# Kernel optimization log

Measured on AMD Instinct MI355X. Metric: run time of the kernel, lower is better.

The kernel has to match this reference:

```python
import jax, jax.numpy as jnp
import numpy as np

N = 100000   # nodes
E = 1000000  # edges
D = 64       # in_features
D_OUT = 64   # out_features


def setup_inputs() -> dict:
    key = jax.random.key(0)
    k1, k2, k3, k4, k5, k6 = jax.random.split(key, 6)
    h = jax.random.normal(k1, (N, D), dtype=jnp.float32)          # current node features ndata['h']
    i = jax.random.normal(k2, (N, D), dtype=jnp.float32)          # initial features ndata['i']
    edge_src = jax.random.randint(k3, (E,), 0, N, dtype=jnp.int32)
    edge_dst = jax.random.randint(k4, (E,), 0, N, dtype=jnp.int32)
    edge_w = jax.random.uniform(k5, (E,), dtype=jnp.float32)      # scalar edge weight edata['x']
    stdv = 1.0 / np.sqrt(D_OUT)
    weight = jax.random.uniform(k6, (2 * D, D_OUT), dtype=jnp.float32,
                                minval=-stdv, maxval=stdv)        # variant=True -> in = 2*D
    return {
        "h": h, "i": i, "weight": weight, "edge_w": edge_w,
        "lamda": jnp.float32(0.5), "alpha": jnp.float32(0.1),
        "edge_src": edge_src, "edge_dst": edge_dst, "layer_idx": 4,
    }


def reference(h, i, weight, edge_w, lamda, alpha, edge_src, edge_dst, layer_idx):
    # theta = min(1, log(lamda/layer_idx + 1))
    theta = jnp.minimum(jnp.float32(1.0), jnp.log(lamda / layer_idx + 1.0))
    # update_all(u_mul_e('h','x','m'), sum('m','h')): edge-weighted gather-scatter SpMM
    m = h[edge_src] * edge_w[:, None]                 # [E, D]
    h_agg = jax.ops.segment_sum(m, edge_dst, num_segments=h.shape[0])  # [N, D]
    # variant=True branch
    support = jnp.concatenate([h_agg, i], axis=1)     # [N, 2D]
    r = (1.0 - alpha) * h_agg + alpha * i             # [N, D]
    out = theta * (support @ weight) + (1.0 - theta) * r
    # residual=True
    out = out + i
    return out
```

## Files before the change

### kernel.cpp

```cpp
#include <hip/hip_runtime.h>
#include <hip/hip_fp16.h>
#include <math.h>


#define DFEAT 64
#define BINSZ 64
#define NBINS 2048
#define CAP   1024
#define CHUNK 2048
#define EPT   4
#define TPB   512

#define ASTR  72

typedef unsigned long long u64;
typedef __attribute__((ext_vector_type(8))) _Float16 f16x8;
typedef __attribute__((ext_vector_type(4))) float f32x4;

__device__ inline unsigned h2u(__half2 h) {
    union { __half2 h; unsigned u; } c; c.h = h; return c.u;
}
__device__ inline __half2 u2h(unsigned u) {
    union { unsigned u; __half2 h; } c; c.u = u; return c.h;
}

__global__ __launch_bounds__(256) void convert_kernel(
    const float* __restrict__ h, const float* __restrict__ weight,
    ushort* __restrict__ h16, ushort* __restrict__ w16,
    int* __restrict__ gcur, int total4) {
    int gid = blockIdx.x * 256 + threadIdx.x;
    int nth = gridDim.x * 256;
    if (gid < NBINS) gcur[gid] = 0;
    for (int i = gid; i < total4; i += nth) {
        float4 v = ((const float4*)h)[i];
        uint2 o;
        o.x = h2u(__floats2half2_rn(v.x, v.y));
        o.y = h2u(__floats2half2_rn(v.z, v.w));
        ((uint2*)h16)[i] = o;
    }
    if (gid < 8192) {
        int j = gid & 7, l = (gid >> 3) & 63, cs = gid >> 9;
        int c = cs >> 2, s = cs & 3, q = l >> 4, m = l & 15;
        w16[gid] = __half_as_ushort(
            __float2half_rn(weight[(s * 32 + q * 8 + j) * DFEAT + c * 16 + m]));
    }
}

__global__ __launch_bounds__(512) void bin_fill_kernel(
    const int* __restrict__ e_src, const int* __restrict__ e_dst,
    const float* __restrict__ e_w, int* __restrict__ gcur,
    u64* __restrict__ bucket, int E) {
    __shared__ int hist[NBINS];
    __shared__ int gbase[NBINS];

    int tid = threadIdx.x;
    int e0 = blockIdx.x * CHUNK;

    for (int i = tid; i < NBINS; i += TPB) hist[i] = 0;
    __syncthreads();

    int d[EPT], s[EPT], r[EPT];
    float w[EPT];
#pragma unroll
    for (int j = 0; j < EPT; ++j) {
        int e = e0 + j * TPB + tid;
        if (e < E) { d[j] = e_dst[e]; s[j] = e_src[e]; w[j] = e_w[e]; }
        else d[j] = -1;
    }
#pragma unroll
    for (int j = 0; j < EPT; ++j)
        if (d[j] >= 0) r[j] = atomicAdd(&hist[d[j] >> 6], 1);
    __syncthreads();

    for (int i = tid; i < NBINS; i += TPB) {
        int c = hist[i];
        gbase[i] = c ? atomicAdd(&gcur[i], c) : 0;
    }
    __syncthreads();

#pragma unroll
    for (int j = 0; j < EPT; ++j) {
        if (d[j] >= 0) {
            int b = d[j] >> 6;
            int pos = gbase[b] + r[j];
            if (pos < CAP) {
                unsigned lo = (unsigned)s[j] | ((unsigned)(d[j] & 63) << 24);
                bucket[(size_t)b * CAP + pos] =
                    ((u64)(unsigned)__float_as_int(w[j]) << 32) | lo;
            }
        }
    }
}

__global__ __launch_bounds__(512) void spmm_kernel(
    const ushort* __restrict__ h16, const u64* __restrict__ bucket,
    const int* __restrict__ gcur, const ushort* __restrict__ w16,
    const float* __restrict__ ifeat,
    const float* __restrict__ lamda_p, const float* __restrict__ alpha_p,
    const int* __restrict__ layer_p,
    float* __restrict__ out, int N) {
    __shared__ u64 sorted[CAP];
    __shared__ __align__(16) ushort agg16[BINSZ * ASTR];
    __shared__ int hist[BINSZ], start[BINSZ];

    int tid = threadIdx.x;
    int bin = blockIdx.x;
    int base = bin << 6;
    int cnt = min(gcur[bin], CAP);
    const u64* bk = bucket + (size_t)bin * CAP;

    if (tid < BINSZ) hist[tid] = 0;
    __syncthreads();

    u64 ev0 = 0, ev1 = 0;
    int dl0 = -1, dl1 = -1, r0 = 0, r1 = 0;
    if (tid < cnt) { ev0 = bk[tid]; dl0 = (int)((ev0 >> 24) & 63); }
    if (tid + TPB < cnt) { ev1 = bk[tid + TPB]; dl1 = (int)((ev1 >> 24) & 63); }
    if (dl0 >= 0) r0 = atomicAdd(&hist[dl0], 1);
    if (dl1 >= 0) r1 = atomicAdd(&hist[dl1], 1);
    __syncthreads();

    if (tid < 64) {
        int v = hist[tid];
        int s = v;
#pragma unroll
        for (int ofs = 1; ofs < 64; ofs <<= 1) {
            int t = __shfl_up(s, ofs);
            if (tid >= ofs) s += t;
        }
        start[tid] = s - v;
    }
    __syncthreads();

    if (dl0 >= 0) sorted[start[dl0] + r0] = ev0;
    if (dl1 >= 0) sorted[start[dl1] + r1] = ev1;
    if (cnt == 0 && tid == 0) sorted[0] = 0;
    __syncthreads();

    int lane = tid & 63, wv = tid >> 6;
    int g8 = lane >> 3;
    int m8 = lane & 7;
    int hf = g8 >> 2;
    int gs = g8 & 3;

    for (int kp = 0; kp < 4; ++kp) {
        int nl = (wv << 3) + (kp << 1) + hf;
        int d = hist[nl];
        int b0 = start[nl];
        int hi = (d > 0) ? (b0 + d - 1) : 0;
        __half2 a0 = u2h(0u), a1 = u2h(0u), a2 = u2h(0u), a3 = u2h(0u);
        for (int t0 = 0; t0 < d; t0 += 16) {
#pragma unroll
            for (int s = 0; s < 4; ++s) {
                int idx = t0 + (s << 2) + gs;
                u64 e = sorted[min(b0 + idx, hi)];
                float wf = (idx < d) ? __int_as_float((int)(e >> 32)) : 0.f;
                __half2 w2 = __float2half2_rn(wf);
                unsigned src = ((unsigned)e) & 0xFFFFFFu;
                uint4 hv = *(const uint4*)(h16 + ((size_t)src << 6) + (m8 << 3));
                a0 = __hfma2(w2, u2h(hv.x), a0);
                a1 = __hfma2(w2, u2h(hv.y), a1);
                a2 = __hfma2(w2, u2h(hv.z), a2);
                a3 = __hfma2(w2, u2h(hv.w), a3);
            }
        }
        a0 = __hadd2(a0, u2h((unsigned)__shfl_xor((int)h2u(a0), 8)));
        a1 = __hadd2(a1, u2h((unsigned)__shfl_xor((int)h2u(a1), 8)));
        a2 = __hadd2(a2, u2h((unsigned)__shfl_xor((int)h2u(a2), 8)));
        a3 = __hadd2(a3, u2h((unsigned)__shfl_xor((int)h2u(a3), 8)));
        a0 = __hadd2(a0, u2h((unsigned)__shfl_xor((int)h2u(a0), 16)));
        a1 = __hadd2(a1, u2h((unsigned)__shfl_xor((int)h2u(a1), 16)));
        a2 = __hadd2(a2, u2h((unsigned)__shfl_xor((int)h2u(a2), 16)));
        a3 = __hadd2(a3, u2h((unsigned)__shfl_xor((int)h2u(a3), 16)));
        if (gs == 0) {
            uint4 o;
            o.x = h2u(a0); o.y = h2u(a1); o.z = h2u(a2); o.w = h2u(a3);
            *(uint4*)(agg16 + nl * ASTR + (m8 << 3)) = o;
        }
    }
    __syncthreads();

    float alf = alpha_p[0];
    float theta = fminf(1.0f, logf(lamda_p[0] / (float)layer_p[0] + 1.0f));
    int m = lane & 15, q = lane >> 4;
    int t = wv >> 1, ch = wv & 1;

    f16x8 faA[2], faI[2];
#pragma unroll
    for (int s = 0; s < 2; ++s)
        faA[s] = *(const f16x8*)(agg16 + (t * 16 + m) * ASTR + s * 32 + q * 8);
    {
        const float* ip = ifeat + (size_t)min(base + t * 16 + m, N - 1) * DFEAT;
#pragma unroll
        for (int s = 0; s < 2; ++s) {
            float4 v0 = *(const float4*)(ip + s * 32 + q * 8);
            float4 v1 = *(const float4*)(ip + s * 32 + q * 8 + 4);
            f16x8 tt;
            tt[0] = (_Float16)v0.x; tt[1] = (_Float16)v0.y;
            tt[2] = (_Float16)v0.z; tt[3] = (_Float16)v0.w;
            tt[4] = (_Float16)v1.x; tt[5] = (_Float16)v1.y;
            tt[6] = (_Float16)v1.z; tt[7] = (_Float16)v1.w;
            faI[s] = tt;
        }
    }

    f32x4 acc[2] = {{0.f, 0.f, 0.f, 0.f}, {0.f, 0.f, 0.f, 0.f}};
#pragma unroll
    for (int ci = 0; ci < 2; ++ci) {
        int c = ch * 2 + ci;
#pragma unroll
        for (int s = 0; s < 2; ++s) {
            f16x8 bA = *(const f16x8*)(w16 + ((c * 4 + s) * 64 + lane) * 8);
            acc[ci] = __builtin_amdgcn_mfma_f32_16x16x32_f16(faA[s], bA, acc[ci], 0, 0, 0);
            f16x8 bI = *(const f16x8*)(w16 + ((c * 4 + s + 2) * 64 + lane) * 8);
            acc[ci] = __builtin_amdgcn_mfma_f32_16x16x32_f16(faI[s], bI, acc[ci], 0, 0, 0);
        }
    }

#pragma unroll
    for (int ci = 0; ci < 2; ++ci) {
        int c = ch * 2 + ci;
        int col = c * 16 + m;
#pragma unroll
        for (int r = 0; r < 4; ++r) {
            int rowL = t * 16 + q * 4 + r;
            int row = base + rowL;
            if (row < N) {
                float av = __half2float(
                    *(const __half*)(agg16 + rowL * ASTR + col));
                float iv = ifeat[(size_t)row * DFEAT + col];
                out[(size_t)row * DFEAT + col] =
                    theta * acc[ci][r] +
                    (1.f - theta) * ((1.f - alf) * av + alf * iv) + iv;
            }
        }
    }
}

extern "C" void kernel_launch(void* const* d_in, const int* in_sizes, int n_in,
                              void* d_out, int out_size, void* d_ws, size_t ws_size,
                              hipStream_t stream) {
    const float* h       = (const float*)d_in[0];
    const float* ifeat   = (const float*)d_in[1];
    const float* weight  = (const float*)d_in[2];
    const float* edge_w  = (const float*)d_in[3];
    const float* lamda_p = (const float*)d_in[4];
    const float* alpha_p = (const float*)d_in[5];
    const int*   e_src   = (const int*)d_in[6];
    const int*   e_dst   = (const int*)d_in[7];
    const int*   layer_p = (const int*)d_in[8];
    float* out = (float*)d_out;

    int N = in_sizes[0] / DFEAT;
    int E = in_sizes[3];
    int nbins = (N + BINSZ - 1) >> 6;

    int* gcur = (int*)d_ws;
    u64* bucket = (u64*)((char*)d_ws + 8192);
    ushort* h16 = (ushort*)((char*)bucket + (size_t)NBINS * CAP * sizeof(u64));
    ushort* w16 = h16 + (size_t)N * DFEAT;

    int total4 = N * DFEAT / 4;
    convert_kernel<<<2048, 256, 0, stream>>>(h, weight, h16, w16, gcur, total4);

    bin_fill_kernel<<<(E + CHUNK - 1) / CHUNK, TPB, 0, stream>>>(
        e_src, e_dst, edge_w, gcur, bucket, E);

    spmm_kernel<<<nbins, TPB, 0, stream>>>(
        h16, bucket, gcur, w16, ifeat, lamda_p, alpha_p, layer_p, out, N);
}
```

Before: 165.8 us.

## Stage binned edges in shared memory and pad global bin counters

The bin fill kernel now does a block-local counting sort: it computes a prefix scan over bin histograms, writes packed edges into a shared staging buffer in bin order, then writes them to the global buckets in that order. Consecutive threads therefore write contiguous bucket slots instead of scattering. The chunk size doubles to 4096 edges per block. Global bin counters are padded to 16 ints apart to reduce atomic contention and false sharing. Edge weights are converted to fp16 at packing time, which removes a per-edge float-to-half conversion in the SpMM loop. The trade-off is a longer block-wide scan with many syncthreads, heavier shared memory use that lowers occupancy, and the 17-bit src packing, which holds only while node ids stay below 131072.

```diff
diff --git a/kernel.cpp b/kernel.cpp
--- a/kernel.cpp
+++ b/kernel.cpp
@@ -7,8 +7,9 @@
 #define BINSZ 64
 #define NBINS 2048
 #define CAP   1024
-#define CHUNK 2048
-#define EPT   4
+#define GPAD  16
+#define CHUNK 4096
+#define EPT   8
 #define TPB   512
 
 #define ASTR  72
@@ -30,7 +31,7 @@
     int* __restrict__ gcur, int total4) {
     int gid = blockIdx.x * 256 + threadIdx.x;
     int nth = gridDim.x * 256;
-    if (gid < NBINS) gcur[gid] = 0;
+    if (gid < NBINS * GPAD) gcur[gid] = 0;
     for (int i = gid; i < total4; i += nth) {
         float4 v = ((const float4*)h)[i];
         uint2 o;
@@ -50,43 +51,80 @@
     const int* __restrict__ e_src, const int* __restrict__ e_dst,
     const float* __restrict__ e_w, int* __restrict__ gcur,
     u64* __restrict__ bucket, int E) {
+    __shared__ u64 staging[CHUNK];
     __shared__ int hist[NBINS];
-    __shared__ int gbase[NBINS];
+    __shared__ ushort offs[NBINS];
+    __shared__ ushort gbase[NBINS];
+    __shared__ int part[TPB];
 
     int tid = threadIdx.x;
     int e0 = blockIdx.x * CHUNK;
+    int cc = min(CHUNK, E - e0);
 
     for (int i = tid; i < NBINS; i += TPB) hist[i] = 0;
     __syncthreads();
 
-    int d[EPT], s[EPT], r[EPT];
-    float w[EPT];
+    int bn[EPT], r[EPT];
+    u64 pk[EPT];
 #pragma unroll
     for (int j = 0; j < EPT; ++j) {
         int e = e0 + j * TPB + tid;
-        if (e < E) { d[j] = e_dst[e]; s[j] = e_src[e]; w[j] = e_w[e]; }
-        else d[j] = -1;
+        bn[j] = -1;
+        if (e < E) {
+            int d = e_dst[e];
+            int src = e_src[e];
+            ushort wb = __half_as_ushort(__float2half_rn(e_w[e]));
+            bn[j] = d >> 6;
+            pk[j] = ((u64)wb << 48) | ((u64)(unsigned)bn[j] << 23) |
+                    ((u64)(unsigned)(d & 63) << 17) | (u64)(unsigned)src;
+        }
     }
 #pragma unroll
     for (int j = 0; j < EPT; ++j)
-        if (d[j] >= 0) r[j] = atomicAdd(&hist[d[j] >> 6], 1);
-    __syncthreads();
+        if (bn[j] >= 0) r[j] = atomicAdd(&hist[bn[j]], 1);
+    __syncthreads();
+
+    int c0 = hist[4 * tid], c1 = hist[4 * tid + 1];
+    int c2 = hist[4 * tid + 2], c3 = hist[4 * tid + 3];
+    int sum = c0 + c1 + c2 + c3;
+    part[tid] = sum;
+    __syncthreads();
+    for (int ofs = 1; ofs < TPB; ofs <<= 1) {
+        int t = (tid >= ofs) ? part[tid - ofs] : 0;
+        __syncthreads();
+        part[tid] += t;
+        __syncthreads();
+    }
+    int excl = part[tid] - sum;
+    offs[4 * tid] = (ushort)excl;
+    offs[4 * tid + 1] = (ushort)(excl + c0);
+    offs[4 * tid + 2] = (ushort)(excl + c0 + c1);
+    offs[4 * tid + 3] = (ushort)(excl + c0 + c1 + c2);
+    __syncthreads();
+
+#pragma unroll
+    for (int j = 0; j < EPT; ++j)
+        if (bn[j] >= 0) staging[offs[bn[j]] + r[j]] = pk[j];
 
     for (int i = tid; i < NBINS; i += TPB) {
         int c = hist[i];
-        gbase[i] = c ? atomicAdd(&gcur[i], c) : 0;
+        int g = c ? atomicAdd(&gcur[i * GPAD], c) : 0;
+        gbase[i] = (ushort)min(g, CAP);
     }
     __syncthreads();
 
 #pragma unroll
     for (int j = 0; j < EPT; ++j) {
-        if (d[j] >= 0) {
-            int b = d[j] >> 6;
-            int pos = gbase[b] + r[j];
+        int p = j * TPB + tid;
+        if (p < cc) {
+            u64 e = staging[p];
+            int bin = (int)((e >> 23) & 2047);
+            int pos = (int)gbase[bin] + (p - (int)offs[bin]);
             if (pos < CAP) {
-                unsigned lo = (unsigned)s[j] | ((unsigned)(d[j] & 63) << 24);
-                bucket[(size_t)b * CAP + pos] =
-                    ((u64)(unsigned)__float_as_int(w[j]) << 32) | lo;
+                unsigned lo = (unsigned)(e & 0x1FFFF) |
+                              (((unsigned)(e >> 17) & 63u) << 24);
+                u64 hi = (e >> 48) << 32;
+                bucket[(size_t)bin * CAP + pos] = hi | lo;
             }
         }
     }
@@ -106,7 +144,7 @@
     int tid = threadIdx.x;
     int bin = blockIdx.x;
     int base = bin << 6;
-    int cnt = min(gcur[bin], CAP);
+    int cnt = min(gcur[bin << 4], CAP);
     const u64* bk = bucket + (size_t)bin * CAP;
 
     if (tid < BINSZ) hist[tid] = 0;
@@ -154,8 +192,8 @@
             for (int s = 0; s < 4; ++s) {
                 int idx = t0 + (s << 2) + gs;
                 u64 e = sorted[min(b0 + idx, hi)];
-                float wf = (idx < d) ? __int_as_float((int)(e >> 32)) : 0.f;
-                __half2 w2 = __float2half2_rn(wf);
+                ushort wb = (idx < d) ? (ushort)(e >> 32) : (ushort)0;
+                __half2 w2 = __half2half2(__ushort_as_half(wb));
                 unsigned src = ((unsigned)e) & 0xFFFFFFu;
                 uint4 hv = *(const uint4*)(h16 + ((size_t)src << 6) + (m8 << 3));
                 a0 = __hfma2(w2, u2h(hv.x), a0);
@@ -256,7 +294,7 @@
     int nbins = (N + BINSZ - 1) >> 6;
 
     int* gcur = (int*)d_ws;
-    u64* bucket = (u64*)((char*)d_ws + 8192);
+    u64* bucket = (u64*)((char*)d_ws + (size_t)NBINS * GPAD * sizeof(int));
     ushort* h16 = (ushort*)((char*)bucket + (size_t)NBINS * CAP * sizeof(u64));
     ushort* w16 = h16 + (size_t)N * DFEAT;
 
```

Result: no change. 164.6 us (-0.7%).

## Presort edges per destination node via global histogram, rank and scan kernels

Applied to the files above, without the earlier changes.

Replaces the bin-level bucketing with a per-node global atomic histogram that records each edge's rank, a per-bin scan, and a fill kernel that writes edges directly in destination-sorted order. The SpMM kernel then just copies the bucket into shared memory instead of re-sorting it with shared atomics. Edge weights are stored as fp16, and the i-feature load is hoisted before the gather loop to overlap latency. The trade-off is many global atomics, an extra rank array round trip and two more launches.

```diff
diff --git a/kernel.cpp b/kernel.cpp
--- a/kernel.cpp
+++ b/kernel.cpp
@@ -7,8 +7,6 @@
 #define BINSZ 64
 #define NBINS 2048
 #define CAP   1024
-#define CHUNK 2048
-#define EPT   4
 #define TPB   512
 
 #define ASTR  72
@@ -27,10 +25,10 @@
 __global__ __launch_bounds__(256) void convert_kernel(
     const float* __restrict__ h, const float* __restrict__ weight,
     ushort* __restrict__ h16, ushort* __restrict__ w16,
-    int* __restrict__ gcur, int total4) {
+    int* __restrict__ node_cnt, int total4) {
     int gid = blockIdx.x * 256 + threadIdx.x;
     int nth = gridDim.x * 256;
-    if (gid < NBINS) gcur[gid] = 0;
+    if (gid < NBINS * BINSZ) node_cnt[gid] = 0;
     for (int i = gid; i < total4; i += nth) {
         float4 v = ((const float4*)h)[i];
         uint2 o;
@@ -46,55 +44,50 @@
     }
 }
 
-__global__ __launch_bounds__(512) void bin_fill_kernel(
+__global__ __launch_bounds__(256) void hist_rank_kernel(
+    const int* __restrict__ e_dst, int* __restrict__ node_cnt,
+    int* __restrict__ rank, int E) {
+    int gid = blockIdx.x * 256 + threadIdx.x;
+    int nth = gridDim.x * 256;
+    for (int e = gid; e < E; e += nth)
+        rank[e] = atomicAdd(&node_cnt[e_dst[e]], 1);
+}
+
+__global__ __launch_bounds__(512) void scan_kernel(
+    const int* __restrict__ node_cnt, int* __restrict__ node_start, int nbins) {
+    int wv = threadIdx.x >> 6, lane = threadIdx.x & 63;
+    int bin = blockIdx.x * 8 + wv;
+    if (bin >= nbins) return;
+    int deg = node_cnt[(bin << 6) + lane];
+    int s = deg;
+#pragma unroll
+    for (int ofs = 1; ofs < 64; ofs <<= 1) {
+        int t = __shfl_up(s, ofs);
+        if (lane >= ofs) s += t;
+    }
+    node_start[(bin << 6) + lane] = s - deg;
+}
+
+__global__ __launch_bounds__(256) void fill_kernel(
     const int* __restrict__ e_src, const int* __restrict__ e_dst,
-    const float* __restrict__ e_w, int* __restrict__ gcur,
-    u64* __restrict__ bucket, int E) {
-    __shared__ int hist[NBINS];
-    __shared__ int gbase[NBINS];
-
-    int tid = threadIdx.x;
-    int e0 = blockIdx.x * CHUNK;
-
-    for (int i = tid; i < NBINS; i += TPB) hist[i] = 0;
-    __syncthreads();
-
-    int d[EPT], s[EPT], r[EPT];
-    float w[EPT];
-#pragma unroll
-    for (int j = 0; j < EPT; ++j) {
-        int e = e0 + j * TPB + tid;
-        if (e < E) { d[j] = e_dst[e]; s[j] = e_src[e]; w[j] = e_w[e]; }
-        else d[j] = -1;
-    }
-#pragma unroll
-    for (int j = 0; j < EPT; ++j)
-        if (d[j] >= 0) r[j] = atomicAdd(&hist[d[j] >> 6], 1);
-    __syncthreads();
-
-    for (int i = tid; i < NBINS; i += TPB) {
-        int c = hist[i];
-        gbase[i] = c ? atomicAdd(&gcur[i], c) : 0;
-    }
-    __syncthreads();
-
-#pragma unroll
-    for (int j = 0; j < EPT; ++j) {
-        if (d[j] >= 0) {
-            int b = d[j] >> 6;
-            int pos = gbase[b] + r[j];
-            if (pos < CAP) {
-                unsigned lo = (unsigned)s[j] | ((unsigned)(d[j] & 63) << 24);
-                bucket[(size_t)b * CAP + pos] =
-                    ((u64)(unsigned)__float_as_int(w[j]) << 32) | lo;
-            }
+    const float* __restrict__ e_w, const int* __restrict__ rank,
+    const int* __restrict__ node_start, u64* __restrict__ bucket, int E) {
+    int gid = blockIdx.x * 256 + threadIdx.x;
+    int nth = gridDim.x * 256;
+    for (int e = gid; e < E; e += nth) {
+        int d = e_dst[e];
+        int pos = node_start[d] + rank[e];
+        if (pos < CAP) {
+            ushort wb = __half_as_ushort(__float2half_rn(e_w[e]));
+            bucket[(size_t)(d >> 6) * CAP + pos] =
+                ((u64)wb << 32) | (u64)(unsigned)e_src[e];
         }
     }
 }
 
 __global__ __launch_bounds__(512) void spmm_kernel(
     const ushort* __restrict__ h16, const u64* __restrict__ bucket,
-    const int* __restrict__ gcur, const ushort* __restrict__ w16,
+    const int* __restrict__ node_cnt, const ushort* __restrict__ w16,
     const float* __restrict__ ifeat,
     const float* __restrict__ lamda_p, const float* __restrict__ alpha_p,
     const int* __restrict__ layer_p,
@@ -102,38 +95,29 @@
     __shared__ u64 sorted[CAP];
     __shared__ __align__(16) ushort agg16[BINSZ * ASTR];
     __shared__ int hist[BINSZ], start[BINSZ];
+    __shared__ int cntS;
 
     int tid = threadIdx.x;
     int bin = blockIdx.x;
     int base = bin << 6;
-    int cnt = min(gcur[bin], CAP);
     const u64* bk = bucket + (size_t)bin * CAP;
 
-    if (tid < BINSZ) hist[tid] = 0;
-    __syncthreads();
-
-    u64 ev0 = 0, ev1 = 0;
-    int dl0 = -1, dl1 = -1, r0 = 0, r1 = 0;
-    if (tid < cnt) { ev0 = bk[tid]; dl0 = (int)((ev0 >> 24) & 63); }
-    if (tid + TPB < cnt) { ev1 = bk[tid + TPB]; dl1 = (int)((ev1 >> 24) & 63); }
-    if (dl0 >= 0) r0 = atomicAdd(&hist[dl0], 1);
-    if (dl1 >= 0) r1 = atomicAdd(&hist[dl1], 1);
-    __syncthreads();
-
     if (tid < 64) {
-        int v = hist[tid];
-        int s = v;
+        int deg = node_cnt[base + tid];
+        int s = deg;
 #pragma unroll
         for (int ofs = 1; ofs < 64; ofs <<= 1) {
             int t = __shfl_up(s, ofs);
             if (tid >= ofs) s += t;
         }
-        start[tid] = s - v;
+        hist[tid] = deg;
+        start[tid] = s - deg;
+        if (tid == 63) cntS = min(s, CAP);
     }
     __syncthreads();
 
-    if (dl0 >= 0) sorted[start[dl0] + r0] = ev0;
-    if (dl1 >= 0) sorted[start[dl1] + r1] = ev1;
+    int cnt = cntS;
+    for (int p = tid; p < cnt; p += TPB) sorted[p] = bk[p];
     if (cnt == 0 && tid == 0) sorted[0] = 0;
     __syncthreads();
 
@@ -143,19 +127,37 @@
     int hf = g8 >> 2;
     int gs = g8 & 3;
 
+    int m = lane & 15, q = lane >> 4;
+    int t = wv >> 1, ch = wv & 1;
+    f16x8 faI[2];
+    {
+        const float* ip = ifeat + (size_t)min(base + t * 16 + m, N - 1) * DFEAT;
+#pragma unroll
+        for (int s = 0; s < 2; ++s) {
+            float4 v0 = *(const float4*)(ip + s * 32 + q * 8);
+            float4 v1 = *(const float4*)(ip + s * 32 + q * 8 + 4);
+            f16x8 tt;
+            tt[0] = (_Float16)v0.x; tt[1] = (_Float16)v0.y;
+            tt[2] = (_Float16)v0.z; tt[3] = (_Float16)v0.w;
+            tt[4] = (_Float16)v1.x; tt[5] = (_Float16)v1.y;
+            tt[6] = (_Float16)v1.z; tt[7] = (_Float16)v1.w;
+            faI[s] = tt;
+        }
+    }
+
     for (int kp = 0; kp < 4; ++kp) {
         int nl = (wv << 3) + (kp << 1) + hf;
         int d = hist[nl];
         int b0 = start[nl];
-        int hi = (d > 0) ? (b0 + d - 1) : 0;
+        int hi = (d > 0) ? min(b0 + d - 1, CAP - 1) : 0;
         __half2 a0 = u2h(0u), a1 = u2h(0u), a2 = u2h(0u), a3 = u2h(0u);
         for (int t0 = 0; t0 < d; t0 += 16) {
 #pragma unroll
             for (int s = 0; s < 4; ++s) {
                 int idx = t0 + (s << 2) + gs;
                 u64 e = sorted[min(b0 + idx, hi)];
-                float wf = (idx < d) ? __int_as_float((int)(e >> 32)) : 0.f;
-                __half2 w2 = __float2half2_rn(wf);
+                ushort wb = (idx < d) ? (ushort)(e >> 32) : (ushort)0;
+                __half2 w2 = __half2half2(__ushort_as_half(wb));
                 unsigned src = ((unsigned)e) & 0xFFFFFFu;
                 uint4 hv = *(const uint4*)(h16 + ((size_t)src << 6) + (m8 << 3));
                 a0 = __hfma2(w2, u2h(hv.x), a0);
@@ -182,27 +184,11 @@
 
     float alf = alpha_p[0];
     float theta = fminf(1.0f, logf(lamda_p[0] / (float)layer_p[0] + 1.0f));
-    int m = lane & 15, q = lane >> 4;
-    int t = wv >> 1, ch = wv & 1;
-
-    f16x8 faA[2], faI[2];
+
+    f16x8 faA[2];
 #pragma unroll
     for (int s = 0; s < 2; ++s)
         faA[s] = *(const f16x8*)(agg16 + (t * 16 + m) * ASTR + s * 32 + q * 8);
-    {
-        const float* ip = ifeat + (size_t)min(base + t * 16 + m, N - 1) * DFEAT;
-#pragma unroll
-        for (int s = 0; s < 2; ++s) {
-            float4 v0 = *(const float4*)(ip + s * 32 + q * 8);
-            float4 v1 = *(const float4*)(ip + s * 32 + q * 8 + 4);
-            f16x8 tt;
-            tt[0] = (_Float16)v0.x; tt[1] = (_Float16)v0.y;
-            tt[2] = (_Float16)v0.z; tt[3] = (_Float16)v0.w;
-            tt[4] = (_Float16)v1.x; tt[5] = (_Float16)v1.y;
-            tt[6] = (_Float16)v1.z; tt[7] = (_Float16)v1.w;
-            faI[s] = tt;
-        }
-    }
 
     f32x4 acc[2] = {{0.f, 0.f, 0.f, 0.f}, {0.f, 0.f, 0.f, 0.f}};
 #pragma unroll
@@ -255,17 +241,23 @@
     int E = in_sizes[3];
     int nbins = (N + BINSZ - 1) >> 6;
 
-    int* gcur = (int*)d_ws;
-    u64* bucket = (u64*)((char*)d_ws + 8192);
+    u64* bucket = (u64*)d_ws;
     ushort* h16 = (ushort*)((char*)bucket + (size_t)NBINS * CAP * sizeof(u64));
     ushort* w16 = h16 + (size_t)N * DFEAT;
+    int* node_cnt = (int*)((char*)w16 + 16384);
+    int* node_start = node_cnt + NBINS * BINSZ;
+    int* rank = node_start + NBINS * BINSZ;
 
     int total4 = N * DFEAT / 4;
-    convert_kernel<<<2048, 256, 0, stream>>>(h, weight, h16, w16, gcur, total4);
-
-    bin_fill_kernel<<<(E + CHUNK - 1) / CHUNK, TPB, 0, stream>>>(
-        e_src, e_dst, edge_w, gcur, bucket, E);
+    convert_kernel<<<2048, 256, 0, stream>>>(h, weight, h16, w16, node_cnt, total4);
+
+    hist_rank_kernel<<<2048, 256, 0, stream>>>(e_dst, node_cnt, rank, E);
+
+    scan_kernel<<<(nbins + 7) / 8, 512, 0, stream>>>(node_cnt, node_start, nbins);
+
+    fill_kernel<<<2048, 256, 0, stream>>>(e_src, e_dst, edge_w, rank,
+                                          node_start, bucket, E);
 
     spmm_kernel<<<nbins, TPB, 0, stream>>>(
-        h16, bucket, gcur, w16, ifeat, lamda_p, alpha_p, layer_p, out, N);
-}
+        h16, bucket, node_cnt, w16, ifeat, lamda_p, alpha_p, layer_p, out, N);
+}
```

Result: slower. 209.5 us (+26.3%).
